# Kernel optimization log

Measured on AMD Instinct MI355X. Metric: run time of the kernel, lower is better.

## Reference

```python
import jax, jax.numpy as jnp
import numpy as np
import math

INPUT_DIM = 1024
DIM_K = 1024
DIM_V = 1024
B, N = 4, 2048

def setup_inputs() -> dict:
    key = jax.random.key(0)
    ks = jax.random.split(key, 7)
    s = 1.0 / math.sqrt(INPUT_DIM)
    return {
        'x':  jax.random.normal(ks[0], (B, N, INPUT_DIM), dtype=jnp.float32),
        'Wq': jax.random.uniform(ks[1], (DIM_K, INPUT_DIM), jnp.float32, -s, s),
        'bq': jax.random.uniform(ks[2], (DIM_K,), jnp.float32, -s, s),
        'Wk': jax.random.uniform(ks[3], (DIM_K, INPUT_DIM), jnp.float32, -s, s),
        'bk': jax.random.uniform(ks[4], (DIM_K,), jnp.float32, -s, s),
        'Wv': jax.random.uniform(ks[5], (DIM_V, INPUT_DIM), jnp.float32, -s, s),
        'bv': jax.random.uniform(ks[6], (DIM_V,), jnp.float32, -s, s),
    }

def reference(x, Wq, bq, Wk, bk, Wv, bv):
    norm_fact = 1.0 / math.sqrt(DIM_K)
    # torch Linear: y = x @ W.T + b
    Q = jnp.einsum('bnd,kd->bnk', x, Wq) + bq  # [B,N,dim_k]
    K = jnp.einsum('bnd,kd->bnk', x, Wk) + bk  # [B,N,dim_k]
    V = jnp.einsum('bnd,vd->bnv', x, Wv) + bv  # [B,N,dim_v]
    scores = jnp.einsum('bqk,bnk->bqn', Q, K)  # [B,N,N]
    # NOTE: original code applies softmax FIRST, then scales by norm_fact
    atten = jax.nn.softmax(scores, axis=-1) * norm_fact
    return jnp.einsum('bqn,bnv->bqv', atten, V)  # [B,N,dim_v]
```

## Files before the change

### kernel.cpp

```cpp
#include <hip/hip_runtime.h>


typedef _Float16 hfx8 __attribute__((ext_vector_type(8)));
typedef _Float16 hfx4 __attribute__((ext_vector_type(4)));
typedef float fx4 __attribute__((ext_vector_type(4)));

__device__ __forceinline__ void load_lds16(const void* g, void* l) {
    __builtin_amdgcn_global_load_lds(
        (const __attribute__((address_space(1))) void*)g,
        (__attribute__((address_space(3))) void*)l, 16, 0, 0);
}

template <int N> __device__ __forceinline__ void vmwait() {
    if constexpr (N == 8) asm volatile("s_waitcnt vmcnt(8)" ::: "memory");
    else asm volatile("s_waitcnt vmcnt(0)" ::: "memory");
}

__device__ __forceinline__ void xcd_remap(int& x, int& y, int& z) {
    const int gx = gridDim.x, gy = gridDim.y;
    const int lin = blockIdx.x + gx * (blockIdx.y + gy * blockIdx.z);
    const int cpx = (gx * gy * gridDim.z) >> 3;
    const int w = (lin & 7) * cpx + (lin >> 3);
    x = w % gx;
    y = (w / gx) % gy;
    z = w / (gx * gy);
}

__global__ __launch_bounds__(256) void conv_all_kernel(
    const float4* __restrict__ x, _Float16* __restrict__ xs,
    const float4* __restrict__ w0, const float4* __restrict__ w1, const float4* __restrict__ w2,
    _Float16* __restrict__ o0, _Float16* __restrict__ o1, _Float16* __restrict__ o2)
{
    const int b = blockIdx.x;
    const float4* in;
    _Float16* out;
    long i;
    if (b < 8192) {
        in = x; out = xs;
        i = (long)b * 256 + threadIdx.x;
    } else {
        const int wi = b - 8192;
        const int wsel = wi >> 10;
        in = wsel == 0 ? w0 : (wsel == 1 ? w1 : w2);
        out = wsel == 0 ? o0 : (wsel == 1 ? o1 : o2);
        i = (long)(wi & 1023) * 256 + threadIdx.x;
    }
    float4 v = in[i];
    hfx4 h;
    h[0] = (_Float16)v.x; h[1] = (_Float16)v.y;
    h[2] = (_Float16)v.z; h[3] = (_Float16)v.w;
    *(hfx4*)&out[i * 4] = h;
}

__global__ __launch_bounds__(256, 2) void gemmQKV(
    const _Float16* __restrict__ A,
    const _Float16* __restrict__ Bq, const _Float16* __restrict__ Bk, const _Float16* __restrict__ Bv,
    const float* __restrict__ bq, const float* __restrict__ bk, const float* __restrict__ bv,
    _Float16* __restrict__ oQ, _Float16* __restrict__ oK, _Float16* __restrict__ oV)
{
    constexpr int BK = 32;
    __shared__ __attribute__((aligned(16))) _Float16 lds[2][4 * 128 * BK];

    int bx, by, zz;
    xcd_remap(bx, by, zz);

    const int tid = threadIdx.x;
    const int lane = tid & 63;
    const int wv = tid >> 6;
    const int wr = wv >> 1, wc = wv & 1;
    const int lr = lane & 15, lk = lane >> 4;

    const long m0 = (long)by * 128;
    const long n0 = (long)bx * 128;

    fx4 acc[3][4][4] = {};

    auto STAGE = [&](int kt, int b) {
#pragma unroll
        for (int i = 0; i < 8; ++i) {
            const int slot = tid & 3;
            if (i < 2) {
                const int row = i * 64 + (tid >> 2);
                load_lds16(A + (m0 + row) * 1024L + kt + ((slot ^ ((row >> 1) & 3)) << 3),
                           &lds[b][row * BK + slot * 8]);
            } else {
                const int which = (i - 2) >> 1;
                const int row = ((i - 2) & 1) * 64 + (tid >> 2);
                const _Float16* Bsel = which == 0 ? Bq : (which == 1 ? Bk : Bv);
                load_lds16(Bsel + (n0 + row) * 1024L + kt + ((slot ^ ((row >> 1) & 3)) << 3),
                           &lds[b][(1 + which) * 4096 + row * BK + slot * 8]);
            }
        }
    };

    const int NT = 1024 / BK;
    STAGE(0, 0);
    STAGE(BK, 1);
    vmwait<8>();
    __builtin_amdgcn_s_barrier();
    __builtin_amdgcn_sched_barrier(0);

    const int rA0 = wr * 64 + lr;
    const int rB0 = wc * 64 + lr;
    const int eA = (((rA0 >> 1) & 3) << 3);
    const int eB = (((rB0 >> 1) & 3) << 3);

    for (int t = 0; t < NT; ++t) {
        const _Float16* L = &lds[t & 1][0];

        hfx8 afr[4];
#pragma unroll
        for (int q = 0; q < 4; ++q)
            afr[q] = *(const hfx8*)&L[(rA0 + q * 16) * BK + ((lk * 8) ^ eA)];

#pragma unroll
        for (int w3 = 0; w3 < 3; ++w3) {
            hfx8 bfr[4];
#pragma unroll
            for (int nf = 0; nf < 4; ++nf)
                bfr[nf] = *(const hfx8*)&L[(1 + w3) * 4096 + (rB0 + nf * 16) * BK + ((lk * 8) ^ eB)];
            __builtin_amdgcn_s_setprio(1);
#pragma unroll
            for (int q = 0; q < 4; ++q)
#pragma unroll
                for (int nf = 0; nf < 4; ++nf)
                    acc[w3][q][nf] = __builtin_amdgcn_mfma_f32_16x16x32_f16(
                        afr[q], bfr[nf], acc[w3][q][nf], 0, 0, 0);
            __builtin_amdgcn_s_setprio(0);
        }

        __builtin_amdgcn_s_barrier();
        if (t + 2 < NT) {
            STAGE((t + 2) * BK, t & 1);
            vmwait<8>();
        } else {
            vmwait<0>();
        }
        __builtin_amdgcn_s_barrier();
        __builtin_amdgcn_sched_barrier(0);
    }

#pragma unroll
    for (int w3 = 0; w3 < 3; ++w3) {
#pragma unroll
        for (int mf = 0; mf < 4; ++mf) {
#pragma unroll
            for (int nf = 0; nf < 4; ++nf) {
                const long row0 = m0 + wr * 64 + mf * 16 + lk * 4;
                const long col = n0 + wc * 64 + nf * 16 + lr;
                if (w3 == 0) {
                    const float bb = bq[col];
#pragma unroll
                    for (int j = 0; j < 4; ++j)
                        oQ[(row0 + j) * 1024 + col] = (_Float16)(acc[0][mf][nf][j] + bb);
                } else if (w3 == 1) {
                    const float bb = bk[col];
#pragma unroll
                    for (int j = 0; j < 4; ++j)
                        oK[(row0 + j) * 1024 + col] = (_Float16)(acc[1][mf][nf][j] + bb);
                } else {
                    const float bb = bv[col];
                    hfx4 pk;
#pragma unroll
                    for (int j = 0; j < 4; ++j) pk[j] = (_Float16)(acc[2][mf][nf][j] + bb);
                    *(hfx4*)&oV[((row0 >> 11) * 1024 + col) * 2048 + (row0 & 2047)] = pk;
                }
            }
        }
    }
}

template <int OMODE>
__global__ __launch_bounds__(256, 2) void gemm2(
    const _Float16* __restrict__ A, const _Float16* __restrict__ Bq,
    float* __restrict__ outF, _Float16* __restrict__ oH,
    int K, int lda, int ldb, int ldc, float alpha,
    long sAz, long sBz, long sCz)
{
    constexpr int BM = 128, BN = 128, BK = 64;
    constexpr int LPT = 8;

    __shared__ __attribute__((aligned(16))) _Float16 lds[2][(BM + BN) * BK];

    int bx, by, z;
    xcd_remap(bx, by, z);

    A += (long)z * sAz;
    const _Float16* B = Bq + (long)z * sBz;

    const int tid = threadIdx.x;
    const int lane = tid & 63;
    const int wv = tid >> 6;
    const int wr = wv >> 1, wc = wv & 1;
    const int lr = lane & 15, lk = lane >> 4;

    const long m0 = (long)by * BM;
    const long n0 = (long)bx * BN;

    fx4 acc[4][4] = {};

    auto STAGE = [&](int kt, int b) {
#pragma unroll
        for (int i = 0; i < LPT; ++i) {
            const int c = i * 256 + tid;
            if (i < 4) {
                const int row = c >> 3, slot = c & 7;
                load_lds16(A + (m0 + row) * (long)lda + kt + ((slot ^ (row & 7)) << 3),
                           &lds[b][c * 8]);
            } else {
                const int c2 = c - 1024;
                const int row = c2 >> 3, slot = c2 & 7;
                load_lds16(B + (n0 + row) * (long)ldb + kt + ((slot ^ (row & 7)) << 3),
                           &lds[b][BM * BK + c2 * 8]);
            }
        }
    };

    const int NT = K / BK;
    STAGE(0, 0);
    STAGE(BK, 1);
    vmwait<8>();
    __builtin_amdgcn_s_barrier();
    __builtin_amdgcn_sched_barrier(0);

    const int rA0 = wr * 64 + lr;
    const int rB0 = wc * 64 + lr;
    const int eA = (rA0 & 7) << 3;
    const int eB = (rB0 & 7) << 3;

    for (int t = 0; t < NT; ++t) {
        const _Float16* LA = &lds[t & 1][0];
        const _Float16* LB = LA + BM * BK;

        hfx8 bfr[4][2];
#pragma unroll
        for (int nf = 0; nf < 4; ++nf)
#pragma unroll
            for (int ks = 0; ks < 2; ++ks)
                bfr[nf][ks] = *(const hfx8*)&LB[(rB0 + nf * 16) * BK + ((ks * 32 + lk * 8) ^ eB)];

#pragma unroll
        for (int q = 0; q < 4; ++q) {
            hfx8 afr[2];
#pragma unroll
            for (int ks = 0; ks < 2; ++ks)
                afr[ks] = *(const hfx8*)&LA[(rA0 + q * 16) * BK + ((ks * 32 + lk * 8) ^ eA)];
            __builtin_amdgcn_s_setprio(1);
#pragma unroll
            for (int nf = 0; nf < 4; ++nf)
#pragma unroll
                for (int ks = 0; ks < 2; ++ks)
                    acc[q][nf] = __builtin_amdgcn_mfma_f32_16x16x32_f16(
                        afr[ks], bfr[nf][ks], acc[q][nf], 0, 0, 0);
            __builtin_amdgcn_s_setprio(0);
        }

        __builtin_amdgcn_s_barrier();
        if (t + 2 < NT) {
            STAGE((t + 2) * BK, t & 1);
            vmwait<8>();
        } else {
            vmwait<0>();
        }
        __builtin_amdgcn_s_barrier();
        __builtin_amdgcn_sched_barrier(0);
    }

#pragma unroll
    for (int mf = 0; mf < 4; ++mf) {
#pragma unroll
        for (int nf = 0; nf < 4; ++nf) {
            const long row0 = m0 + wr * 64 + mf * 16 + lk * 4;
            const long col = n0 + wc * 64 + nf * 16 + lr;
            if constexpr (OMODE == 0) {
                float* oz = outF + (long)z * sCz;
#pragma unroll
                for (int j = 0; j < 4; ++j)
                    oz[(row0 + j) * (long)ldc + col] = alpha * acc[mf][nf][j];
            } else {
                _Float16* oz = oH + (long)z * sCz;
#pragma unroll
                for (int j = 0; j < 4; ++j)
                    oz[(row0 + j) * (long)ldc + col] = (_Float16)(alpha * acc[mf][nf][j]);
            }
        }
    }
}

__global__ __launch_bounds__(256) void softmax_kernel(_Float16* __restrict__ S)
{
    const long row = blockIdx.x;
    _Float16* r = S + row * 2048;
    const int t = threadIdx.x;

    const hfx8 hv = *(const hfx8*)&r[t * 8];
    float v[8];
#pragma unroll
    for (int j = 0; j < 8; ++j) v[j] = (float)hv[j];

    float mx = v[0];
#pragma unroll
    for (int j = 1; j < 8; ++j) mx = fmaxf(mx, v[j]);
#pragma unroll
    for (int o = 32; o; o >>= 1) mx = fmaxf(mx, __shfl_xor(mx, o, 64));

    __shared__ float redm[4];
    __shared__ float reds[4];
    const int w = t >> 6;
    if ((t & 63) == 0) redm[w] = mx;
    __syncthreads();
    mx = fmaxf(fmaxf(redm[0], redm[1]), fmaxf(redm[2], redm[3]));

    float e[8];
    float s = 0.f;
#pragma unroll
    for (int j = 0; j < 8; ++j) {
        e[j] = __expf(v[j] - mx);
        s += e[j];
    }
#pragma unroll
    for (int o = 32; o; o >>= 1) s += __shfl_xor(s, o, 64);
    if ((t & 63) == 0) reds[w] = s;
    __syncthreads();
    s = reds[0] + reds[1] + reds[2] + reds[3];

    const float inv = 1.0f / s;
    hfx8 p;
#pragma unroll
    for (int j = 0; j < 8; ++j) p[j] = (_Float16)(e[j] * inv);
    *(hfx8*)&r[t * 8] = p;
}

extern "C" void kernel_launch(void* const* d_in, const int* in_sizes, int n_in,
                              void* d_out, int out_size, void* d_ws, size_t ws_size,
                              hipStream_t stream)
{
    const float* x  = (const float*)d_in[0];
    const float* Wq = (const float*)d_in[1];
    const float* bq = (const float*)d_in[2];
    const float* Wk = (const float*)d_in[3];
    const float* bk = (const float*)d_in[4];
    const float* Wv = (const float*)d_in[5];
    const float* bv = (const float*)d_in[6];
    float* out = (float*)d_out;

    _Float16* xs  = (_Float16*)d_ws;
    _Float16* Wqh = xs + 8192ull * 1024;
    _Float16* Wkh = Wqh + 1024ull * 1024;
    _Float16* Wvh = Wkh + 1024ull * 1024;
    _Float16* Qp  = Wvh + 1024ull * 1024;
    _Float16* Ks  = Qp + 8192ull * 1024;
    _Float16* Vt  = Ks + 8192ull * 1024;
    _Float16* Sh  = Vt + 4ull * 1024 * 2048;

    dim3 blk(256);

    conv_all_kernel<<<11264, blk, 0, stream>>>(
        (const float4*)x, xs,
        (const float4*)Wq, (const float4*)Wk, (const float4*)Wv, Wqh, Wkh, Wvh);

    gemmQKV<<<dim3(8, 64, 1), blk, 0, stream>>>(
        xs, Wqh, Wkh, Wvh, bq, bk, bv, Qp, Ks, Vt);

    gemm2<2><<<dim3(16, 16, 4), blk, 0, stream>>>(
        Qp, Ks, nullptr, Sh,
        1024, 1024, 1024, 2048, 1.0f,
        2097152L, 2097152L, 4194304L);

    softmax_kernel<<<2048 * 4, blk, 0, stream>>>(Sh);

    gemm2<0><<<dim3(8, 16, 4), blk, 0, stream>>>(
        Sh, Vt, out, nullptr,
        2048, 2048, 2048, 1024, 0.03125f,
        4194304L, 2097152L, 2097152L);
}
```

Measured before the change: 156.7 us.

## Widen batched GEMM tiles to 128x256 with BK=32 for scores and PV

Replaces the 128x128x64 batched GEMM with a 128x256 tile at BK=32, so each block reuses one A fragment set across two B sub-tiles and the accumulators double to 128 fp32 per thread. This is meant to raise arithmetic intensity and cut redundant loads of A, and it halves the grid for both the QK^T and PV GEMMs. In exchange it adds register pressure (occupancy hint of 2 may spill or limit waves), leaves fewer blocks to fill the CUs, and doubles the number of K iterations with barriers. Also hardcodes NT=32 in the QKV kernel, which is equivalent.

```diff
diff --git a/kernel.cpp b/kernel.cpp
--- a/kernel.cpp
+++ b/kernel.cpp
@@ -13,6 +13,7 @@
 
 template <int N> __device__ __forceinline__ void vmwait() {
     if constexpr (N == 8) asm volatile("s_waitcnt vmcnt(8)" ::: "memory");
+    else if constexpr (N == 6) asm volatile("s_waitcnt vmcnt(6)" ::: "memory");
     else asm volatile("s_waitcnt vmcnt(0)" ::: "memory");
 }
 
@@ -93,7 +94,7 @@
         }
     };
 
-    const int NT = 1024 / BK;
+    const int NT = 32;
     STAGE(0, 0);
     STAGE(BK, 1);
     vmwait<8>();
@@ -171,22 +172,20 @@
 }
 
 template <int OMODE>
-__global__ __launch_bounds__(256, 2) void gemm2(
-    const _Float16* __restrict__ A, const _Float16* __restrict__ Bq,
+__global__ __launch_bounds__(256, 2) void gemmS(
+    const _Float16* __restrict__ A, const _Float16* __restrict__ B0,
     float* __restrict__ outF, _Float16* __restrict__ oH,
     int K, int lda, int ldb, int ldc, float alpha,
     long sAz, long sBz, long sCz)
 {
-    constexpr int BM = 128, BN = 128, BK = 64;
-    constexpr int LPT = 8;
-
-    __shared__ __attribute__((aligned(16))) _Float16 lds[2][(BM + BN) * BK];
+    constexpr int BK = 32;
+    __shared__ __attribute__((aligned(16))) _Float16 lds[2][384 * BK];
 
     int bx, by, z;
     xcd_remap(bx, by, z);
 
     A += (long)z * sAz;
-    const _Float16* B = Bq + (long)z * sBz;
+    const _Float16* B = B0 + (long)z * sBz;
 
     const int tid = threadIdx.x;
     const int lane = tid & 63;
@@ -194,24 +193,25 @@
     const int wr = wv >> 1, wc = wv & 1;
     const int lr = lane & 15, lk = lane >> 4;
 
-    const long m0 = (long)by * BM;
-    const long n0 = (long)bx * BN;
-
-    fx4 acc[4][4] = {};
+    const long m0 = (long)by * 128;
+    const long n0 = (long)bx * 256;
+
+    fx4 acc[2][4][4] = {};
 
     auto STAGE = [&](int kt, int b) {
 #pragma unroll
-        for (int i = 0; i < LPT; ++i) {
+        for (int i = 0; i < 6; ++i) {
             const int c = i * 256 + tid;
-            if (i < 4) {
-                const int row = c >> 3, slot = c & 7;
-                load_lds16(A + (m0 + row) * (long)lda + kt + ((slot ^ (row & 7)) << 3),
-                           &lds[b][c * 8]);
+            const int slot = c & 3;
+            if (i < 2) {
+                const int row = c >> 2;
+                load_lds16(A + (m0 + row) * (long)lda + kt + ((slot ^ ((row >> 1) & 3)) << 3),
+                           &lds[b][row * BK + slot * 8]);
             } else {
-                const int c2 = c - 1024;
-                const int row = c2 >> 3, slot = c2 & 7;
-                load_lds16(B + (n0 + row) * (long)ldb + kt + ((slot ^ (row & 7)) << 3),
-                           &lds[b][BM * BK + c2 * 8]);
+                const int c2 = c - 512;
+                const int row = c2 >> 2;
+                load_lds16(B + (n0 + row) * (long)ldb + kt + ((slot ^ ((row >> 1) & 3)) << 3),
+                           &lds[b][4096 + row * BK + slot * 8]);
             }
         }
     };
@@ -219,46 +219,43 @@
     const int NT = K / BK;
     STAGE(0, 0);
     STAGE(BK, 1);
-    vmwait<8>();
+    vmwait<6>();
     __builtin_amdgcn_s_barrier();
     __builtin_amdgcn_sched_barrier(0);
 
     const int rA0 = wr * 64 + lr;
     const int rB0 = wc * 64 + lr;
-    const int eA = (rA0 & 7) << 3;
-    const int eB = (rB0 & 7) << 3;
+    const int eA = (((rA0 >> 1) & 3) << 3);
+    const int eB = (((rB0 >> 1) & 3) << 3);
 
     for (int t = 0; t < NT; ++t) {
-        const _Float16* LA = &lds[t & 1][0];
-        const _Float16* LB = LA + BM * BK;
-
-        hfx8 bfr[4][2];
-#pragma unroll
-        for (int nf = 0; nf < 4; ++nf)
-#pragma unroll
-            for (int ks = 0; ks < 2; ++ks)
-                bfr[nf][ks] = *(const hfx8*)&LB[(rB0 + nf * 16) * BK + ((ks * 32 + lk * 8) ^ eB)];
-
-#pragma unroll
-        for (int q = 0; q < 4; ++q) {
-            hfx8 afr[2];
-#pragma unroll
-            for (int ks = 0; ks < 2; ++ks)
-                afr[ks] = *(const hfx8*)&LA[(rA0 + q * 16) * BK + ((ks * 32 + lk * 8) ^ eA)];
+        const _Float16* L = &lds[t & 1][0];
+
+        hfx8 afr[4];
+#pragma unroll
+        for (int q = 0; q < 4; ++q)
+            afr[q] = *(const hfx8*)&L[(rA0 + q * 16) * BK + ((lk * 8) ^ eA)];
+
+#pragma unroll
+        for (int s = 0; s < 2; ++s) {
+            hfx8 bfr[4];
+#pragma unroll
+            for (int nf = 0; nf < 4; ++nf)
+                bfr[nf] = *(const hfx8*)&L[4096 + s * 4096 + (rB0 + nf * 16) * BK + ((lk * 8) ^ eB)];
             __builtin_amdgcn_s_setprio(1);
 #pragma unroll
-            for (int nf = 0; nf < 4; ++nf)
-#pragma unroll
-                for (int ks = 0; ks < 2; ++ks)
-                    acc[q][nf] = __builtin_amdgcn_mfma_f32_16x16x32_f16(
-                        afr[ks], bfr[nf][ks], acc[q][nf], 0, 0, 0);
+            for (int q = 0; q < 4; ++q)
+#pragma unroll
+                for (int nf = 0; nf < 4; ++nf)
+                    acc[s][q][nf] = __builtin_amdgcn_mfma_f32_16x16x32_f16(
+                        afr[q], bfr[nf], acc[s][q][nf], 0, 0, 0);
             __builtin_amdgcn_s_setprio(0);
         }
 
         __builtin_amdgcn_s_barrier();
         if (t + 2 < NT) {
             STAGE((t + 2) * BK, t & 1);
-            vmwait<8>();
+            vmwait<6>();
         } else {
             vmwait<0>();
         }
@@ -267,21 +264,24 @@
     }
 
 #pragma unroll
-    for (int mf = 0; mf < 4; ++mf) {
-#pragma unroll
-        for (int nf = 0; nf < 4; ++nf) {
-            const long row0 = m0 + wr * 64 + mf * 16 + lk * 4;
-            const long col = n0 + wc * 64 + nf * 16 + lr;
-            if constexpr (OMODE == 0) {
-                float* oz = outF + (long)z * sCz;
-#pragma unroll
-                for (int j = 0; j < 4; ++j)
-                    oz[(row0 + j) * (long)ldc + col] = alpha * acc[mf][nf][j];
-            } else {
-                _Float16* oz = oH + (long)z * sCz;
-#pragma unroll
-                for (int j = 0; j < 4; ++j)
-                    oz[(row0 + j) * (long)ldc + col] = (_Float16)(alpha * acc[mf][nf][j]);
+    for (int s = 0; s < 2; ++s) {
+#pragma unroll
+        for (int mf = 0; mf < 4; ++mf) {
+#pragma unroll
+            for (int nf = 0; nf < 4; ++nf) {
+                const long row0 = m0 + wr * 64 + mf * 16 + lk * 4;
+                const long col = n0 + s * 128 + wc * 64 + nf * 16 + lr;
+                if constexpr (OMODE == 0) {
+                    float* oz = outF + (long)z * sCz;
+#pragma unroll
+                    for (int j = 0; j < 4; ++j)
+                        oz[(row0 + j) * (long)ldc + col] = alpha * acc[s][mf][nf][j];
+                } else {
+                    _Float16* oz = oH + (long)z * sCz;
+#pragma unroll
+                    for (int j = 0; j < 4; ++j)
+                        oz[(row0 + j) * (long)ldc + col] = (_Float16)(alpha * acc[s][mf][nf][j]);
+                }
             }
         }
     }
@@ -362,14 +362,14 @@
     gemmQKV<<<dim3(8, 64, 1), blk, 0, stream>>>(
         xs, Wqh, Wkh, Wvh, bq, bk, bv, Qp, Ks, Vt);
 
-    gemm2<2><<<dim3(16, 16, 4), blk, 0, stream>>>(
+    gemmS<2><<<dim3(8, 16, 4), blk, 0, stream>>>(
         Qp, Ks, nullptr, Sh,
         1024, 1024, 1024, 2048, 1.0f,
         2097152L, 2097152L, 4194304L);
 
     softmax_kernel<<<2048 * 4, blk, 0, stream>>>(Sh);
 
-    gemm2<0><<<dim3(8, 16, 4), blk, 0, stream>>>(
+    gemmS<0><<<dim3(4, 16, 4), blk, 0, stream>>>(
         Sh, Vt, out, nullptr,
         2048, 2048, 2048, 1024, 0.03125f,
         4194304L, 2097152L, 2097152L);
```

Result: slower. 168.7 us (+7.7%).
